# Optimization experiments

Measured on AMD Instinct MI355X. Metric: run time of the kernel, lower is better.

## Reference

```python
import jax, jax.numpy as jnp
import numpy as np
from jax import lax

N_CLASS = 21
K_ED = 5
ALPHA = 0.1
BN_EPS = 1e-5


def _conv(x, w):
    # NCHW conv, stride 1, SAME padding
    return lax.conv_general_dilated(x, w, (1, 1), 'SAME',
                                    dimension_numbers=('NCHW', 'OIHW', 'NCHW'))


def _bn(x, g, b, m, v):
    # inference-mode BatchNorm2d with running stats
    scale = (g * lax.rsqrt(v + BN_EPS))[None, :, None, None]
    return (x - m[None, :, None, None]) * scale + b[None, :, None, None]


def _maxpool(x, k):
    return lax.reduce_window(x, -jnp.inf, lax.max, (1, 1, k, k), (1, 1, 1, 1), 'SAME')


def setup_inputs() -> dict:
    key = jax.random.key(0)
    ks = jax.random.split(key, 12)
    N, F, H, W, C = 8, 512, 96, 96, N_CLASS
    feature = jax.random.normal(ks[0], (N, F, H, W), jnp.float32)
    global_pred = jax.random.normal(ks[1], (N, C, H, W), jnp.float32)
    conv1_w = jax.random.normal(ks[2], (256, F, 3, 3), jnp.float32) * 0.02
    bn1_g = jnp.ones((256,), jnp.float32)
    bn1_b = jnp.zeros((256,), jnp.float32)
    bn1_m = jax.random.normal(ks[3], (256,), jnp.float32) * 0.1
    bn1_v = jax.random.uniform(ks[4], (256,), jnp.float32, 0.5, 1.5)
    conv2_w = jax.random.normal(ks[5], (128, 256, 3, 3), jnp.float32) * 0.02
    bn2_g = jnp.ones((128,), jnp.float32)
    bn2_b = jnp.zeros((128,), jnp.float32)
    bn2_m = jax.random.normal(ks[6], (128,), jnp.float32) * 0.1
    bn2_v = jax.random.uniform(ks[7], (128,), jnp.float32, 0.5, 1.5)
    conv3_w = jax.random.normal(ks[8], (C, 128, 1, 1), jnp.float32) * 0.02
    conv3_b = jnp.zeros((C,), jnp.float32)
    return dict(feature=feature, global_pred=global_pred,
                conv1_w=conv1_w, bn1_g=bn1_g, bn1_b=bn1_b, bn1_m=bn1_m, bn1_v=bn1_v,
                conv2_w=conv2_w, bn2_g=bn2_g, bn2_b=bn2_b, bn2_m=bn2_m, bn2_v=bn2_v,
                conv3_w=conv3_w, conv3_b=conv3_b)


def reference(feature, global_pred, conv1_w, bn1_g, bn1_b, bn1_m, bn1_v,
              conv2_w, bn2_g, bn2_b, bn2_m, bn2_v, conv3_w, conv3_b):
    N, F, H, W = feature.shape
    # hard labels -> one-hot [N, C, H, W]
    lbl = jnp.argmax(global_pred, axis=1)
    onehot = jnp.transpose(jax.nn.one_hot(lbl, N_CLASS, dtype=feature.dtype), (0, 3, 1, 2))
    # binary morphology: dilation = max-pool, erosion = -max-pool(-x)
    d = _maxpool(onehot, K_ED)
    e = -_maxpool(-onehot, K_ED)
    transition = jnp.sum(d - e, axis=1, keepdims=True)
    transition = jnp.where(transition >= 1.0, 1.0, transition)  # [N,1,H,W]
    tfeat = feature * transition
    # per-class masked mean over ALL H*W pixels (faithful to .mean(dim=2))
    objs = jnp.einsum('nfhw,nchw->ncf', feature, e) / (H * W)  # [N,C,F]
    # cdist(p=2) between transition-feature pixels and class prototypes
    x = tfeat.reshape(N, F, H * W).transpose(0, 2, 1)  # [N,HW,F]
    x2 = jnp.sum(x * x, axis=-1, keepdims=True)
    o2 = jnp.sum(objs * objs, axis=-1)
    d2 = jnp.maximum(x2 + o2[:, None, :] - 2.0 * jnp.einsum('npf,ncf->npc', x, objs), 0.0)
    cd = jnp.where(d2 > 0, jnp.sqrt(jnp.where(d2 > 0, d2, 1.0)), 0.0)  # safe sqrt
    dist = 1.0 - jax.nn.softmax(cd, axis=-1)  # [N,HW,C]
    obj_feat = jnp.einsum('npc,ncf->nfp', dist, objs).reshape(N, F, H, W)
    fusion = (feature * (1.0 - transition)
              + feature * transition * ALPHA
              + obj_feat * transition * (1.0 - ALPHA))
    # fusion_predictor: convBNReLU -> bilinear x2 -> convBNReLU -> 1x1 conv
    h = jax.nn.relu(_bn(_conv(fusion, conv1_w), bn1_g, bn1_b, bn1_m, bn1_v))
    h = jax.image.resize(h, (N, 256, 2 * H, 2 * W), method='bilinear')
    h = jax.nn.relu(_bn(_conv(h, conv2_w), bn2_g, bn2_b, bn2_m, bn2_v))
    logits = _conv(h, conv3_w) + conv3_b[None, :, None, None]
    # eval mode: softmax over classes
    return jax.nn.softmax(logits, axis=1)
```

## Files before the change

### kernel.cpp

```cpp
#include <hip/hip_runtime.h>
#include <cstdint>
#include <cstddef>

typedef __attribute__((ext_vector_type(4))) float f32x4;
typedef __attribute__((ext_vector_type(8))) short short8;

__device__ __forceinline__ float bf2f(unsigned short u) {
  union { unsigned int i; float f; } x; x.i = ((unsigned int)u) << 16; return x.f;
}
__device__ __forceinline__ unsigned short f2bf(float f) {
  union { float f; unsigned int i; } x; x.f = f;
  unsigned int r = x.i + 0x7fffu + ((x.i >> 16) & 1u);
  return (unsigned short)(r >> 16);
}
__device__ __forceinline__ void gload16(unsigned short* lds, const unsigned short* g) {
  __builtin_amdgcn_global_load_lds(
      (const __attribute__((address_space(1))) unsigned int*)g,
      (__attribute__((address_space(3))) unsigned int*)lds, 16, 0, 0);
}

__global__ void k_prepbn(const float* __restrict__ g1, const float* __restrict__ b1,
                         const float* __restrict__ m1, const float* __restrict__ v1,
                         const float* __restrict__ g2, const float* __restrict__ b2,
                         const float* __restrict__ m2, const float* __restrict__ v2,
                         float* __restrict__ s1, float* __restrict__ bb1,
                         float* __restrict__ s2, float* __restrict__ bb2) {
  int i = threadIdx.x;
  if (i < 256) { float s = g1[i] * rsqrtf(v1[i] + 1e-5f); s1[i] = s; bb1[i] = b1[i] - m1[i] * s; }
  if (i < 128) { float s = g2[i] * rsqrtf(v2[i] + 1e-5f); s2[i] = s; bb2[i] = b2[i] - m2[i] * s; }
}

__global__ void k_prepw1(const float* __restrict__ w, unsigned short* __restrict__ wt) {
  int i = blockIdx.x * 256 + threadIdx.x;
  int o = i / 4608, k = i - o * 4608;
  int cblk = k / 288, r = k - cblk * 288;
  int t = r >> 5, cl = r & 31;
  int ci = cblk * 32 + cl;
  int ty = t / 3, tx = t - ty * 3;
  wt[i] = f2bf(w[((o * 512 + ci) * 3 + ty) * 3 + tx]);
}
__global__ void k_prepw2(const float* __restrict__ w, unsigned short* __restrict__ wt) {
  int i = blockIdx.x * 256 + threadIdx.x;
  int o = i / 2304, k = i - o * 2304;
  int cblk = k / 288, r = k - cblk * 288;
  int t = r >> 5, cl = r & 31;
  int ci = cblk * 32 + cl;
  int ty = t / 3, tx = t - ty * 3;
  wt[i] = f2bf(w[((o * 256 + ci) * 3 + ty) * 3 + tx]);
}
__global__ void k_prepw3(const float* __restrict__ w3, unsigned short* __restrict__ w3b) {
  int i = blockIdx.x * 256 + threadIdx.x;
  int c = i >> 7, k = i & 127;
  w3b[i] = (c < 21) ? f2bf(w3[c * 128 + k]) : (unsigned short)0;
}

template <int HP, int WP, int C>
__global__ void k_border(unsigned short* __restrict__ p) {
  const int B = 2 * WP + 2 * (HP - 2);
  const int total = 8 * B * (C / 8);
  int i = blockIdx.x * 256 + threadIdx.x;
  if (i >= total) return;
  const int cg = i % (C / 8);
  int b = i / (C / 8);
  const int n = b / B; b -= n * B;
  int y, x;
  if (b < WP) { y = 0; x = b; }
  else if (b < 2 * WP) { y = HP - 1; x = b - WP; }
  else { int r = b - 2 * WP; y = 1 + (r >> 1); x = (r & 1) ? (WP - 1) : 0; }
  short8 z = {0, 0, 0, 0, 0, 0, 0, 0};
  *(short8*)&p[(((long)n * HP + y) * WP + x) * C + cg * 8] = z;
}

__global__ __launch_bounds__(256)
void k_featT(const float* __restrict__ feat, unsigned short* __restrict__ featT) {
  const int g = blockIdx.x * 256 + threadIdx.x;
  const int n = g / 9216, p = g - n * 9216;
  const int fg0 = blockIdx.y * 16;
  const float* src = feat + (long)n * 512 * 9216 + p;
  unsigned short* dst = featT + ((long)n * 9216 + p) * 512;
  for (int fg = fg0; fg < fg0 + 16; fg++) {
    short8 o;
    #pragma unroll
    for (int j = 0; j < 8; j++) o[j] = (short)f2bf(src[(long)(fg * 8 + j) * 9216]);
    *(short8*)&dst[fg * 8] = o;
  }
}

__global__ void k_labels(const float* __restrict__ gp, signed char* __restrict__ lab) {
  int p = blockIdx.x * 256 + threadIdx.x;
  int n = p / 9216, q = p - n * 9216;
  const float* g = gp + (long)n * 21 * 9216 + q;
  float best = g[0]; int bi = 0;
  #pragma unroll
  for (int c = 1; c < 21; c++) {
    float v = g[(long)c * 9216];
    if (v > best) { best = v; bi = c; }
  }
  lab[p] = (signed char)bi;
}

__global__ void k_em(const signed char* __restrict__ lab, signed char* __restrict__ em) {
  int p = blockIdx.x * 256 + threadIdx.x;
  int n = p / 9216, q = p - n * 9216, y = q / 96, x = q - y * 96;
  const signed char* L = lab + n * 9216;
  signed char l0 = L[q];
  bool uni = true;
  for (int dy = -2; dy <= 2; dy++) {
    int yy = y + dy; if (yy < 0 || yy > 95) continue;
    for (int dx = -2; dx <= 2; dx++) {
      int xx = x + dx; if (xx < 0 || xx > 95) continue;
      uni = uni && (L[yy * 96 + xx] == l0);
    }
  }
  em[p] = uni ? l0 : (signed char)-1;
}

__global__ __launch_bounds__(256)
void k_objsT(const unsigned short* __restrict__ featT, const signed char* __restrict__ em,
             float* __restrict__ objs) {
  __shared__ float part[21 * 512];
  __shared__ signed char emL[256];
  __shared__ int pres[21];
  const int b = blockIdx.x;
  const int n = b / 36;
  const int px0 = (b - n * 36) * 256;
  const int tid = threadIdx.x;
  for (int i = tid; i < 21 * 512; i += 256) part[i] = 0.f;
  if (tid < 21) pres[tid] = 0;
  emL[tid] = em[n * 9216 + px0 + tid];
  __syncthreads();
  const unsigned short* base = featT + ((long)n * 9216 + px0) * 512 + tid * 2;
  for (int px = 0; px < 256; px++) {
    const int c0 = emL[px];
    if (c0 >= 0) {
      if (tid == 0) pres[c0] = 1;
      unsigned int v = *(const unsigned int*)&base[(long)px * 512];
      atomicAdd(&part[c0 * 512 + tid * 2], bf2f((unsigned short)(v & 0xffff)));
      atomicAdd(&part[c0 * 512 + tid * 2 + 1], bf2f((unsigned short)(v >> 16)));
    }
  }
  __syncthreads();
  for (int i = tid; i < 21 * 512; i += 256) {
    const int c = i >> 9;
    if (pres[c]) atomicAdd(&objs[(long)n * 21 * 512 + i], part[i] * (1.0f / 9216.0f));
  }
}

__global__ void k_objfin(const float* __restrict__ objs, float* __restrict__ o2,
                         unsigned short* __restrict__ oc) {
  const int b = blockIdx.x;
  const int n = b >> 5, c = b & 31;
  const int lane = threadIdx.x;
  unsigned short* dst = oc + ((long)n * 32 + c) * 512;
  if (c < 21) {
    const float* o = objs + ((long)n * 21 + c) * 512;
    float s = 0.f;
    for (int f = lane; f < 512; f += 64) {
      float v = o[f];
      s += v * v;
      dst[f] = f2bf(v);
    }
    #pragma unroll
    for (int off = 32; off; off >>= 1) s += __shfl_down(s, off);
    if (lane == 0) o2[n * 21 + c] = s;
  } else {
    for (int f = lane; f < 512; f += 64) dst[f] = 0;
  }
}

__global__ __launch_bounds__(256)
void k_dist_mfma(const unsigned short* __restrict__ featT,
                 const unsigned short* __restrict__ objs_c,
                 const float* __restrict__ o2, float* __restrict__ dist) {
  const int n = blockIdx.y;
  const int w = threadIdx.x >> 6, lane = threadIdx.x & 63;
  const int lrow = lane & 15, kg = lane >> 4;
  const int px = blockIdx.x * 64 + w * 16 + lrow;
  const unsigned short* fb = featT + ((long)n * 9216 + px) * 512 + kg * 8;
  const unsigned short* a0p = objs_c + ((long)n * 32 + lrow) * 512 + kg * 8;
  const unsigned short* a1p = a0p + 16 * 512;
  f32x4 acc0 = {0.f, 0.f, 0.f, 0.f}, acc1 = {0.f, 0.f, 0.f, 0.f};
  float x2 = 0.f;
  #pragma unroll
  for (int s = 0; s < 16; s++) {
    const short8 b = *(const short8*)&fb[s * 32];
    const short8 a0 = *(const short8*)&a0p[s * 32];
    const short8 a1 = *(const short8*)&a1p[s * 32];
    acc0 = __builtin_amdgcn_mfma_f32_16x16x32_bf16(a0, b, acc0, 0, 0, 0);
    acc1 = __builtin_amdgcn_mfma_f32_16x16x32_bf16(a1, b, acc1, 0, 0, 0);
    #pragma unroll
    for (int j = 0; j < 8; j++) { float v = bf2f((unsigned short)b[j]); x2 += v * v; }
  }
  x2 += __shfl_xor(x2, 16); x2 += __shfl_xor(x2, 32);
  float cd[8], mx = -1e30f;
  #pragma unroll
  for (int r = 0; r < 4; r++) {
    const int c = kg * 4 + r;
    float d2 = x2 + o2[n * 21 + c] - 2.f * acc0[r];
    cd[r] = sqrtf(fmaxf(d2, 0.f)); mx = fmaxf(mx, cd[r]);
  }
  #pragma unroll
  for (int r = 0; r < 4; r++) {
    const int c = 16 + kg * 4 + r;
    if (c < 21) {
      float d2 = x2 + o2[n * 21 + c] - 2.f * acc1[r];
      cd[4 + r] = sqrtf(fmaxf(d2, 0.f)); mx = fmaxf(mx, cd[4 + r]);
    } else cd[4 + r] = -1e30f;
  }
  mx = fmaxf(mx, __shfl_xor(mx, 16)); mx = fmaxf(mx, __shfl_xor(mx, 32));
  float sum = 0.f;
  #pragma unroll
  for (int k = 0; k < 8; k++) {
    cd[k] = (cd[k] > -1e29f) ? __expf(cd[k] - mx) : 0.f;
    sum += cd[k];
  }
  sum += __shfl_xor(sum, 16); sum += __shfl_xor(sum, 32);
  const float inv = 1.f / sum;
  #pragma unroll
  for (int r = 0; r < 4; r++)
    dist[((long)n * 21 + kg * 4 + r) * 9216 + px] = 1.f - cd[r] * inv;
  #pragma unroll
  for (int r = 0; r < 4; r++) {
    const int c = 16 + kg * 4 + r;
    if (c < 21) dist[((long)n * 21 + c) * 9216 + px] = 1.f - cd[4 + r] * inv;
  }
}

__global__ __launch_bounds__(256)
void k_fusion(const unsigned short* __restrict__ featT, const signed char* __restrict__ em,
              const float* __restrict__ dist, const float* __restrict__ objs,
              unsigned short* __restrict__ fuP) {
  __shared__ float ob[21 * 512];
  __shared__ float dl[64][21];
  __shared__ signed char eml[64];
  const int blk = blockIdx.x;
  const int n = blk / 144;
  const int p0 = (blk - n * 144) * 64;
  const int tid = threadIdx.x;
  for (int i = tid; i < 21 * 512; i += 256) ob[i] = objs[(long)n * 21 * 512 + i];
  for (int i = tid; i < 64 * 21; i += 256) {
    int px = i & 63, c = i >> 6;
    dl[px][c] = dist[((long)n * 21 + c) * 9216 + p0 + px];
  }
  if (tid < 64) eml[tid] = em[n * 9216 + p0 + tid];
  __syncthreads();
  const int px = tid & 63;
  const int fg = (tid >> 6) * 8;
  const int q = p0 + px;
  const int y = q / 96, x = q - y * 96;
  unsigned short* dst = fuP + (((long)n * 98 + y + 1) * 98 + (x + 1)) * 512;
  const bool t = eml[px] < 0;
  const unsigned short* srcT = featT + ((long)n * 9216 + q) * 512;
  for (int f0 = 0; f0 < 512; f0 += 32) {
    short8 o;
    const short8 fvv = *(const short8*)&srcT[f0 + fg];
    #pragma unroll
    for (int j = 0; j < 8; j++) {
      const int f = f0 + fg + j;
      float fv = bf2f((unsigned short)fvv[j]);
      if (t) {
        float of = 0.f;
        #pragma unroll
        for (int c = 0; c < 21; c++) of += dl[px][c] * ob[c * 512 + f];
        fv = 0.1f * fv + 0.9f * of;
      }
      o[j] = (short)f2bf(fv);
    }
    *(short8*)&dst[fg] = o;
    dst += 32;
  }
}

template <int CIN, int NK>
__global__ __launch_bounds__(256)
void conv3x3_gemm(const unsigned short* __restrict__ inP,
                  const unsigned short* __restrict__ wT,
                  const float* __restrict__ scale, const float* __restrict__ bias,
                  unsigned short* __restrict__ out,
                  int Hout, int Wout, int Hp, int Wp, int COUT, int nbN) {
  __shared__ unsigned short ldsA[3][4096];
  __shared__ unsigned short ldsB[3][4096];
  const int tid = threadIdx.x;
  const int chunk = gridDim.x >> 3;
  const int bid = (blockIdx.x & 7) * chunk + (blockIdx.x >> 3);
  const int mb = bid / nbN, nb = bid - mb * nbN;
  const int bm0 = mb * 128, bn0 = nb * 128;
  const int KT = 9 * CIN;
  const int HWo = Hout * Wout;

  const int rA = tid >> 2;
  const int ch8 = (((tid & 3) ^ ((tid >> 3) & 3)) * 8);
  const int m0 = bm0 + rA, m1 = m0 + 64;
  const int n0 = m0 / HWo; const int q0 = m0 - n0 * HWo;
  const int y0 = q0 / Wout, x0 = q0 - y0 * Wout;
  const int n1 = m1 / HWo; const int q1 = m1 - n1 * HWo;
  const int y1 = q1 / Wout, x1 = q1 - y1 * Wout;
  const unsigned short* gA0 = inP + ((long)(n0 * Hp + y0) * Wp + x0) * CIN + ch8;
  const unsigned short* gA1 = inP + ((long)(n1 * Hp + y1) * Wp + x1) * CIN + ch8;
  const unsigned short* gB0 = wT + (long)(bn0 + rA) * KT + ch8;
  const unsigned short* gB1 = wT + (long)(bn0 + rA + 64) * KT + ch8;

  const int lane = tid & 63;
  const int wv = tid >> 6;
  const int wr = wv >> 1, wc = wv & 1;
  const int lrow = lane & 15, kg = lane >> 4;
  const int arow = wr * 64 + lrow;
  const int aoff = arow * 32 + (kg ^ ((arow >> 1) & 3)) * 8;
  const int brow = wc * 64 + lrow;
  const int boff = brow * 32 + (kg ^ ((brow >> 1) & 3)) * 8;

  f32x4 acc[4][4];
  const f32x4 zero = {0.f, 0.f, 0.f, 0.f};
  #pragma unroll
  for (int i = 0; i < 4; i++)
    #pragma unroll
    for (int j = 0; j < 4; j++) acc[i][j] = zero;

  auto stage = [&](int b, int s) {
    const int cblk = s / 9;
    const int t = s - cblk * 9;
    const int ty = t / 3, tx = t - ty * 3;
    const long offA = (long)(ty * Wp + tx) * CIN + cblk * 32;
    gload16(&ldsA[b][tid * 8], gA0 + offA);
    gload16(&ldsA[b][2048 + tid * 8], gA1 + offA);
    const long k0 = (long)s * 32;
    gload16(&ldsB[b][tid * 8], gB0 + k0);
    gload16(&ldsB[b][2048 + tid * 8], gB1 + k0);
  };

  auto kstep = [&](int rd) {
    const unsigned short* A = ldsA[rd];
    const unsigned short* B = ldsB[rd];
    short8 af[4], bfr[4];
    #pragma unroll
    for (int i = 0; i < 4; i++) af[i] = *(const short8*)&A[aoff + i * 512];
    #pragma unroll
    for (int j = 0; j < 4; j++) bfr[j] = *(const short8*)&B[boff + j * 512];
    __builtin_amdgcn_s_setprio(1);
    #pragma unroll
    for (int i = 0; i < 4; i++)
      #pragma unroll
      for (int j = 0; j < 4; j++)
        acc[i][j] = __builtin_amdgcn_mfma_f32_16x16x32_bf16(af[i], bfr[j], acc[i][j], 0, 0, 0);
    __builtin_amdgcn_s_setprio(0);
  };

  stage(0, 0);
  stage(1, 1);
  int rd = 0, prev = 2;
  for (int s = 0; s < NK - 2; ++s) {
    __builtin_amdgcn_s_barrier();
    asm volatile("" ::: "memory");
    stage(prev, s + 2);
    asm volatile("s_waitcnt vmcnt(8)" ::: "memory");
    __builtin_amdgcn_s_barrier();
    asm volatile("" ::: "memory");
    kstep(rd);
    prev = rd; rd = (rd == 2) ? 0 : rd + 1;
  }
  asm volatile("s_waitcnt vmcnt(4)" ::: "memory");
  __builtin_amdgcn_s_barrier();
  asm volatile("" ::: "memory");
  kstep(rd);
  rd = (rd == 2) ? 0 : rd + 1;
  asm volatile("s_waitcnt vmcnt(0)" ::: "memory");
  __builtin_amdgcn_s_barrier();
  asm volatile("" ::: "memory");
  kstep(rd);

  #pragma unroll
  for (int i = 0; i < 4; i++) {
    const int row = bm0 + wr * 64 + i * 16 + kg * 4;
    #pragma unroll
    for (int j = 0; j < 4; j++) {
      const int col = bn0 + wc * 64 + j * 16 + lrow;
      const float sc = scale[col], bi = bias[col];
      #pragma unroll
      for (int r = 0; r < 4; r++) {
        float v = acc[i][j][r] * sc + bi;
        v = v > 0.f ? v : 0.f;
        out[(long)(row + r) * COUT + col] = f2bf(v);
      }
    }
  }
}

__global__ __launch_bounds__(256)
void conv2_fused(const unsigned short* __restrict__ inP,
                 const unsigned short* __restrict__ wT,
                 const float* __restrict__ scale, const float* __restrict__ bias,
                 const unsigned short* __restrict__ w3b, const float* __restrict__ b3,
                 float* __restrict__ out) {
  constexpr int CIN = 256, NK = 72;
  constexpr int Wout = 192, Hp = 194, Wp = 194;
  constexpr int HWo = 192 * 192;
  constexpr int KT = 9 * CIN;
  __shared__ unsigned short pool[6 * 4096];
  const int tid = threadIdx.x;
  const int chunk = gridDim.x >> 3;
  const int bid = (blockIdx.x & 7) * chunk + (blockIdx.x >> 3);
  const int bm0 = bid * 128;

  const int rA = tid >> 2;
  const int ch8 = (((tid & 3) ^ ((tid >> 3) & 3)) * 8);
  const int m0 = bm0 + rA, m1 = m0 + 64;
  const int n0 = m0 / HWo; const int q0 = m0 - n0 * HWo;
  const int y0 = q0 / Wout, x0 = q0 - y0 * Wout;
  const int n1 = m1 / HWo; const int q1 = m1 - n1 * HWo;
  const int y1 = q1 / Wout, x1 = q1 - y1 * Wout;
  const unsigned short* gA0 = inP + ((long)(n0 * Hp + y0) * Wp + x0) * CIN + ch8;
  const unsigned short* gA1 = inP + ((long)(n1 * Hp + y1) * Wp + x1) * CIN + ch8;
  const unsigned short* gB0 = wT + (long)rA * KT + ch8;
  const unsigned short* gB1 = wT + (long)(rA + 64) * KT + ch8;

  const int lane = tid & 63;
  const int wv = tid >> 6;
  const int wr = wv >> 1, wc = wv & 1;
  const int lrow = lane & 15, kg = lane >> 4;
  const int arow = wr * 64 + lrow;
  const int aoff = arow * 32 + (kg ^ ((arow >> 1) & 3)) * 8;
  const int brow = wc * 64 + lrow;
  const int boff = brow * 32 + (kg ^ ((brow >> 1) & 3)) * 8;

  f32x4 acc[4][4];
  const f32x4 zero = {0.f, 0.f, 0.f, 0.f};
  #pragma unroll
  for (int i = 0; i < 4; i++)
    #pragma unroll
    for (int j = 0; j < 4; j++) acc[i][j] = zero;

  auto stage = [&](int b, int s) {
    const int cblk = s / 9;
    const int t = s - cblk * 9;
    const int ty = t / 3, tx = t - ty * 3;
    const long offA = (long)(ty * Wp + tx) * CIN + cblk * 32;
    gload16(&pool[b * 4096 + tid * 8], gA0 + offA);
    gload16(&pool[b * 4096 + 2048 + tid * 8], gA1 + offA);
    const long k0 = (long)s * 32;
    gload16(&pool[12288 + b * 4096 + tid * 8], gB0 + k0);
    gload16(&pool[12288 + b * 4096 + 2048 + tid * 8], gB1 + k0);
  };

  auto kstep = [&](int rd) {
    const unsigned short* A = &pool[rd * 4096];
    const unsigned short* B = &pool[12288 + rd * 4096];
    short8 af[4], bfr[4];
    #pragma unroll
    for (int i = 0; i < 4; i++) af[i] = *(const short8*)&A[aoff + i * 512];
    #pragma unroll
    for (int j = 0; j < 4; j++) bfr[j] = *(const short8*)&B[boff + j * 512];
    __builtin_amdgcn_s_setprio(1);
    #pragma unroll
    for (int i = 0; i < 4; i++)
      #pragma unroll
      for (int j = 0; j < 4; j++)
        acc[i][j] = __builtin_amdgcn_mfma_f32_16x16x32_bf16(af[i], bfr[j], acc[i][j], 0, 0, 0);
    __builtin_amdgcn_s_setprio(0);
  };

  stage(0, 0);
  stage(1, 1);
  int rd = 0;
  for (int s = 0; s < NK; ++s) {
    if (s < NK - 1)
      asm volatile("s_waitcnt vmcnt(4)" ::: "memory");
    else
      asm volatile("s_waitcnt vmcnt(0)" ::: "memory");
    __builtin_amdgcn_s_barrier();
    asm volatile("" ::: "memory");
    kstep(rd);
    if (s + 2 < NK) stage((rd + 2 >= 3) ? rd - 1 : rd + 2, s + 2);
    rd = (rd == 2) ? 0 : rd + 1;
  }

  asm volatile("s_waitcnt lgkmcnt(0)" ::: "memory");
  __builtin_amdgcn_s_barrier();
  asm volatile("" ::: "memory");
  #pragma unroll
  for (int j = 0; j < 4; j++) {
    const int ch = wc * 64 + j * 16 + lrow;
    const float sc = scale[ch], bi = bias[ch];
    #pragma unroll
    for (int i = 0; i < 4; i++) {
      const int pxb = wr * 64 + i * 16 + kg * 4;
      #pragma unroll
      for (int r = 0; r < 4; r++) {
        const int px = pxb + r;
        float v = acc[i][j][r] * sc + bi;
        v = v > 0.f ? v : 0.f;
        pool[px * 128 + (ch ^ ((px & 7) << 3))] = f2bf(v);
      }
    }
  }
  asm volatile("s_waitcnt lgkmcnt(0)" ::: "memory");
  __builtin_amdgcn_s_barrier();
  asm volatile("" ::: "memory");

  #pragma unroll
  for (int g = 0; g < 2; g++) {
    const int px = wv * 32 + g * 16 + lrow;
    f32x4 acc0 = {0.f, 0.f, 0.f, 0.f}, acc1 = {0.f, 0.f, 0.f, 0.f};
    #pragma unroll
    for (int s = 0; s < 4; s++) {
      const int ch0 = s * 32 + kg * 8;
      const short8 b = *(const short8*)&pool[px * 128 + (ch0 ^ ((px & 7) << 3))];
      const short8 a0 = *(const short8*)&w3b[lrow * 128 + ch0];
      const short8 a1 = *(const short8*)&w3b[(16 + lrow) * 128 + ch0];
      acc0 = __builtin_amdgcn_mfma_f32_16x16x32_bf16(a0, b, acc0, 0, 0, 0);
      acc1 = __builtin_amdgcn_mfma_f32_16x16x32_bf16(a1, b, acc1, 0, 0, 0);
    }
    float lg[8], mx = -1e30f;
    #pragma unroll
    for (int r = 0; r < 4; r++) {
      lg[r] = acc0[r] + b3[kg * 4 + r];
      mx = fmaxf(mx, lg[r]);
    }
    #pragma unroll
    for (int r = 0; r < 4; r++) {
      const int c = 16 + kg * 4 + r;
      if (c < 21) { lg[4 + r] = acc1[r] + b3[c]; mx = fmaxf(mx, lg[4 + r]); }
      else lg[4 + r] = -1e30f;
    }
    mx = fmaxf(mx, __shfl_xor(mx, 16)); mx = fmaxf(mx, __shfl_xor(mx, 32));
    float sum = 0.f;
    #pragma unroll
    for (int k = 0; k < 8; k++) {
      lg[k] = (lg[k] > -1e29f) ? __expf(lg[k] - mx) : 0.f;
      sum += lg[k];
    }
    sum += __shfl_xor(sum, 16); sum += __shfl_xor(sum, 32);
    const float inv = 1.f / sum;
    const int m = bm0 + px;
    const int n = m / HWo;
    const int q = m - n * HWo;
    #pragma unroll
    for (int r = 0; r < 4; r++)
      out[((long)n * 21 + kg * 4 + r) * (long)HWo + q] = lg[r] * inv;
    #pragma unroll
    for (int r = 0; r < 4; r++) {
      const int c = 16 + kg * 4 + r;
      if (c < 21) out[((long)n * 21 + c) * (long)HWo + q] = lg[4 + r] * inv;
    }
  }
}

__global__ void k_upsample(const unsigned short* __restrict__ h1,
                           unsigned short* __restrict__ h2P) {
  const int idx = blockIdx.x * 256 + threadIdx.x;
  const int c8 = (idx & 31) * 8;
  const int p = idx >> 5;
  const int n = p / 36864; const int rr = p - n * 36864;
  const int Y = rr / 192, X = rr - Y * 192;
  const int ky = Y >> 1, kx = X >> 1;
  int yA, yB, xA, xB; float wyA, wyB, wxA, wxB;
  if ((Y & 1) == 0) { yA = ky > 0 ? ky - 1 : 0; yB = ky; wyA = 0.25f; wyB = 0.75f; }
  else { yA = ky; yB = ky < 95 ? ky + 1 : 95; wyA = 0.75f; wyB = 0.25f; }
  if ((X & 1) == 0) { xA = kx > 0 ? kx - 1 : 0; xB = kx; wxA = 0.25f; wxB = 0.75f; }
  else { xA = kx; xB = kx < 95 ? kx + 1 : 95; wxA = 0.75f; wxB = 0.25f; }
  const unsigned short* hb = h1 + (long)n * 96 * 96 * 256 + c8;
  const short8 vaa = *(const short8*)&hb[((long)yA * 96 + xA) * 256];
  const short8 vab = *(const short8*)&hb[((long)yA * 96 + xB) * 256];
  const short8 vba = *(const short8*)&hb[((long)yB * 96 + xA) * 256];
  const short8 vbb = *(const short8*)&hb[((long)yB * 96 + xB) * 256];
  short8 o;
  #pragma unroll
  for (int j = 0; j < 8; j++) {
    float v = wyA * (wxA * bf2f((unsigned short)vaa[j]) + wxB * bf2f((unsigned short)vab[j])) +
              wyB * (wxA * bf2f((unsigned short)vba[j]) + wxB * bf2f((unsigned short)vbb[j]));
    o[j] = (short)f2bf(v);
  }
  *(short8*)&h2P[(((long)n * 194 + Y + 1) * 194 + X + 1) * 256 + c8] = o;
}

extern "C" void kernel_launch(void* const* d_in, const int* in_sizes, int n_in,
                              void* d_out, int out_size, void* d_ws, size_t ws_size,
                              hipStream_t stream) {
  const float* feature = (const float*)d_in[0];
  const float* gp = (const float*)d_in[1];
  const float* w1 = (const float*)d_in[2];
  const float* g1 = (const float*)d_in[3];
  const float* b1 = (const float*)d_in[4];
  const float* m1 = (const float*)d_in[5];
  const float* v1 = (const float*)d_in[6];
  const float* w2 = (const float*)d_in[7];
  const float* g2 = (const float*)d_in[8];
  const float* b2 = (const float*)d_in[9];
  const float* m2 = (const float*)d_in[10];
  const float* v2 = (const float*)d_in[11];
  const float* w3 = (const float*)d_in[12];
  const float* b3 = (const float*)d_in[13];
  float* out = (float*)d_out;

  char* ws = (char*)d_ws;
  size_t off = 0;
  auto alloc = [&](size_t bytes) -> void* {
    void* p = ws + off;
    off += (bytes + 255) & ~(size_t)255;
    return p;
  };
  signed char* lab = (signed char*)alloc(73728);
  signed char* em = (signed char*)alloc(73728);
  float* objs = (float*)alloc(8 * 21 * 512 * 4);
  float* o2 = (float*)alloc(168 * 4);
  unsigned short* objs_c = (unsigned short*)alloc((size_t)8 * 32 * 512 * 2);
  float* dist = (float*)alloc((size_t)8 * 21 * 9216 * 4);
  unsigned short* w1t = (unsigned short*)alloc((size_t)256 * 4608 * 2);
  unsigned short* w2t = (unsigned short*)alloc((size_t)128 * 2304 * 2);
  unsigned short* w3b = (unsigned short*)alloc((size_t)32 * 128 * 2);
  float* s1 = (float*)alloc(256 * 4);
  float* bb1 = (float*)alloc(256 * 4);
  float* s2 = (float*)alloc(128 * 4);
  float* bb2 = (float*)alloc(128 * 4);
  const size_t fuP_bytes = (size_t)8 * 98 * 98 * 512 * 2;
  unsigned short* fuP = (unsigned short*)alloc(fuP_bytes);
  const size_t h1_bytes = (size_t)8 * 96 * 96 * 256 * 2;
  unsigned short* h1 = (unsigned short*)alloc(h1_bytes);
  const size_t h2P_bytes = (size_t)8 * 194 * 194 * 256 * 2;
  unsigned short* h2P = (unsigned short*)alloc(h2P_bytes);
  unsigned short* featT = h2P;

  if (off > ws_size) return;

  k_prepbn<<<1, 256, 0, stream>>>(g1, b1, m1, v1, g2, b2, m2, v2, s1, bb1, s2, bb2);
  k_prepw1<<<4608, 256, 0, stream>>>(w1, w1t);
  k_prepw2<<<1152, 256, 0, stream>>>(w2, w2t);
  k_prepw3<<<16, 256, 0, stream>>>(w3, w3b);

  k_border<98, 98, 512><<<777, 256, 0, stream>>>(fuP);
  hipMemsetAsync(objs, 0, 8 * 21 * 512 * 4, stream);

  k_labels<<<288, 256, 0, stream>>>(gp, lab);
  k_em<<<288, 256, 0, stream>>>(lab, em);
  k_featT<<<dim3(288, 4), 256, 0, stream>>>(feature, featT);
  k_objsT<<<288, 256, 0, stream>>>(featT, em, objs);
  k_objfin<<<256, 64, 0, stream>>>(objs, o2, objs_c);
  k_dist_mfma<<<dim3(144, 8), 256, 0, stream>>>(featT, objs_c, o2, dist);
  k_fusion<<<1152, 256, 0, stream>>>(featT, em, dist, objs, fuP);

  conv3x3_gemm<512, 144><<<1152, 256, 0, stream>>>(fuP, w1t, s1, bb1, h1,
                                                   96, 96, 98, 98, 256, 2);
  k_border<194, 194, 256><<<772, 256, 0, stream>>>(h2P);
  k_upsample<<<36864, 256, 0, stream>>>(h1, h2P);
  conv2_fused<<<2304, 256, 0, stream>>>(h2P, w2t, s2, bb2, w3b, b3, out);
}
```

Before: 765.3 us.

## Fuse prep, border, label, objs and dist/fusion kernels to cut launches and traffic

Merges the weight, BN and border prep kernels into single multi-role launches. The prototype accumulation moves into the feature-transpose pass, so the transposed bf16 features are not reread, and it accumulates from fp32 values instead of bf16. The distance softmax is computed inside the fusion kernel, which drops the global dist buffer round-trip. Upsample also zeros the padded border. This reduces launch count and memory traffic, at the cost of extra per-block shared-memory loads of objs and heavier LDS atomics in the transpose.

```diff
diff --git a/kernel.cpp b/kernel.cpp
--- a/kernel.cpp
+++ b/kernel.cpp
@@ -19,84 +19,74 @@
       (__attribute__((address_space(3))) unsigned int*)lds, 16, 0, 0);
 }
 
-__global__ void k_prepbn(const float* __restrict__ g1, const float* __restrict__ b1,
-                         const float* __restrict__ m1, const float* __restrict__ v1,
-                         const float* __restrict__ g2, const float* __restrict__ b2,
-                         const float* __restrict__ m2, const float* __restrict__ v2,
-                         float* __restrict__ s1, float* __restrict__ bb1,
-                         float* __restrict__ s2, float* __restrict__ bb2) {
-  int i = threadIdx.x;
-  if (i < 256) { float s = g1[i] * rsqrtf(v1[i] + 1e-5f); s1[i] = s; bb1[i] = b1[i] - m1[i] * s; }
-  if (i < 128) { float s = g2[i] * rsqrtf(v2[i] + 1e-5f); s2[i] = s; bb2[i] = b2[i] - m2[i] * s; }
-}
-
-__global__ void k_prepw1(const float* __restrict__ w, unsigned short* __restrict__ wt) {
-  int i = blockIdx.x * 256 + threadIdx.x;
-  int o = i / 4608, k = i - o * 4608;
-  int cblk = k / 288, r = k - cblk * 288;
-  int t = r >> 5, cl = r & 31;
-  int ci = cblk * 32 + cl;
-  int ty = t / 3, tx = t - ty * 3;
-  wt[i] = f2bf(w[((o * 512 + ci) * 3 + ty) * 3 + tx]);
-}
-__global__ void k_prepw2(const float* __restrict__ w, unsigned short* __restrict__ wt) {
-  int i = blockIdx.x * 256 + threadIdx.x;
-  int o = i / 2304, k = i - o * 2304;
-  int cblk = k / 288, r = k - cblk * 288;
-  int t = r >> 5, cl = r & 31;
-  int ci = cblk * 32 + cl;
-  int ty = t / 3, tx = t - ty * 3;
-  wt[i] = f2bf(w[((o * 256 + ci) * 3 + ty) * 3 + tx]);
-}
-__global__ void k_prepw3(const float* __restrict__ w3, unsigned short* __restrict__ w3b) {
-  int i = blockIdx.x * 256 + threadIdx.x;
-  int c = i >> 7, k = i & 127;
-  w3b[i] = (c < 21) ? f2bf(w3[c * 128 + k]) : (unsigned short)0;
-}
-
-template <int HP, int WP, int C>
-__global__ void k_border(unsigned short* __restrict__ p) {
-  const int B = 2 * WP + 2 * (HP - 2);
-  const int total = 8 * B * (C / 8);
-  int i = blockIdx.x * 256 + threadIdx.x;
-  if (i >= total) return;
-  const int cg = i % (C / 8);
-  int b = i / (C / 8);
-  const int n = b / B; b -= n * B;
-  int y, x;
-  if (b < WP) { y = 0; x = b; }
-  else if (b < 2 * WP) { y = HP - 1; x = b - WP; }
-  else { int r = b - 2 * WP; y = 1 + (r >> 1); x = (r & 1) ? (WP - 1) : 0; }
-  short8 z = {0, 0, 0, 0, 0, 0, 0, 0};
-  *(short8*)&p[(((long)n * HP + y) * WP + x) * C + cg * 8] = z;
-}
-
-__global__ __launch_bounds__(256)
-void k_featT(const float* __restrict__ feat, unsigned short* __restrict__ featT) {
-  const int g = blockIdx.x * 256 + threadIdx.x;
-  const int n = g / 9216, p = g - n * 9216;
-  const int fg0 = blockIdx.y * 16;
-  const float* src = feat + (long)n * 512 * 9216 + p;
-  unsigned short* dst = featT + ((long)n * 9216 + p) * 512;
-  for (int fg = fg0; fg < fg0 + 16; fg++) {
-    short8 o;
-    #pragma unroll
-    for (int j = 0; j < 8; j++) o[j] = (short)f2bf(src[(long)(fg * 8 + j) * 9216]);
-    *(short8*)&dst[fg * 8] = o;
-  }
-}
-
-__global__ void k_labels(const float* __restrict__ gp, signed char* __restrict__ lab) {
-  int p = blockIdx.x * 256 + threadIdx.x;
-  int n = p / 9216, q = p - n * 9216;
-  const float* g = gp + (long)n * 21 * 9216 + q;
-  float best = g[0]; int bi = 0;
-  #pragma unroll
-  for (int c = 1; c < 21; c++) {
-    float v = g[(long)c * 9216];
-    if (v > best) { best = v; bi = c; }
-  }
-  lab[p] = (signed char)bi;
+__global__ void k_prep(const float* __restrict__ w1, const float* __restrict__ w2,
+                       const float* __restrict__ w3,
+                       const float* __restrict__ g1, const float* __restrict__ b1,
+                       const float* __restrict__ m1, const float* __restrict__ v1,
+                       const float* __restrict__ g2, const float* __restrict__ b2,
+                       const float* __restrict__ m2, const float* __restrict__ v2,
+                       unsigned short* __restrict__ w1t, unsigned short* __restrict__ w2t,
+                       unsigned short* __restrict__ w3b,
+                       float* __restrict__ s1, float* __restrict__ bb1,
+                       float* __restrict__ s2, float* __restrict__ bb2) {
+  const int blk = blockIdx.x;
+  const int tid = threadIdx.x;
+  if (blk < 4608) {
+    int i = blk * 256 + tid;
+    int o = i / 4608, k = i - o * 4608;
+    int cblk = k / 288, r = k - cblk * 288;
+    int t = r >> 5, cl = r & 31;
+    int ci = cblk * 32 + cl;
+    int ty = t / 3, tx = t - ty * 3;
+    w1t[i] = f2bf(w1[((o * 512 + ci) * 3 + ty) * 3 + tx]);
+  } else if (blk < 5760) {
+    int i = (blk - 4608) * 256 + tid;
+    int o = i / 2304, k = i - o * 2304;
+    int cblk = k / 288, r = k - cblk * 288;
+    int t = r >> 5, cl = r & 31;
+    int ci = cblk * 32 + cl;
+    int ty = t / 3, tx = t - ty * 3;
+    w2t[i] = f2bf(w2[((o * 256 + ci) * 3 + ty) * 3 + tx]);
+  } else if (blk < 5776) {
+    int i = (blk - 5760) * 256 + tid;
+    int c = i >> 7, k = i & 127;
+    w3b[i] = (c < 21) ? f2bf(w3[c * 128 + k]) : (unsigned short)0;
+  } else {
+    if (tid < 256) { float s = g1[tid] * rsqrtf(v1[tid] + 1e-5f); s1[tid] = s; bb1[tid] = b1[tid] - m1[tid] * s; }
+    if (tid < 128) { float s = g2[tid] * rsqrtf(v2[tid] + 1e-5f); s2[tid] = s; bb2[tid] = b2[tid] - m2[tid] * s; }
+  }
+}
+
+__global__ void k_labels_init(const float* __restrict__ gp, signed char* __restrict__ lab,
+                              unsigned short* __restrict__ fuP, float* __restrict__ objs) {
+  const int blk = blockIdx.x;
+  const int tid = threadIdx.x;
+  if (blk < 288) {
+    int p = blk * 256 + tid;
+    int n = p / 9216, q = p - n * 9216;
+    const float* g = gp + (long)n * 21 * 9216 + q;
+    float best = g[0]; int bi = 0;
+    #pragma unroll
+    for (int c = 1; c < 21; c++) {
+      float v = g[(long)c * 9216];
+      if (v > best) { best = v; bi = c; }
+    }
+    lab[p] = (signed char)bi;
+  } else if (blk < 1064) {
+    int i = (blk - 288) * 256 + tid;
+    const int B = 2 * 98 + 2 * 96;
+    const int cg = i & 63; int b = i >> 6;
+    const int n = b / B; b -= n * B;
+    int y, x;
+    if (b < 98) { y = 0; x = b; }
+    else if (b < 196) { y = 97; x = b - 98; }
+    else { int r = b - 196; y = 1 + (r >> 1); x = (r & 1) ? 97 : 0; }
+    short8 z = {0, 0, 0, 0, 0, 0, 0, 0};
+    *(short8*)&fuP[(((long)n * 98 + y) * 98 + x) * 512 + cg * 8] = z;
+  } else {
+    int i = (blk - 1064) * 256 + tid;
+    objs[i] = 0.f;
+  }
 }
 
 __global__ void k_em(const signed char* __restrict__ lab, signed char* __restrict__ em) {
@@ -116,33 +106,42 @@
 }
 
 __global__ __launch_bounds__(256)
-void k_objsT(const unsigned short* __restrict__ featT, const signed char* __restrict__ em,
-             float* __restrict__ objs) {
-  __shared__ float part[21 * 512];
-  __shared__ signed char emL[256];
+void k_featT_objs(const float* __restrict__ feat, const signed char* __restrict__ em,
+                  unsigned short* __restrict__ featT, float* __restrict__ objs) {
+  __shared__ float part[21 * 128];
   __shared__ int pres[21];
-  const int b = blockIdx.x;
-  const int n = b / 36;
-  const int px0 = (b - n * 36) * 256;
+  const int g = blockIdx.x * 256 + threadIdx.x;
+  const int n = g / 9216, p = g - n * 9216;
+  const int fg0 = blockIdx.y * 16;
   const int tid = threadIdx.x;
-  for (int i = tid; i < 21 * 512; i += 256) part[i] = 0.f;
+  for (int i = tid; i < 21 * 128; i += 256) part[i] = 0.f;
   if (tid < 21) pres[tid] = 0;
-  emL[tid] = em[n * 9216 + px0 + tid];
   __syncthreads();
-  const unsigned short* base = featT + ((long)n * 9216 + px0) * 512 + tid * 2;
-  for (int px = 0; px < 256; px++) {
-    const int c0 = emL[px];
+  const int c0 = em[g];
+  if (c0 >= 0) pres[c0] = 1;
+  const float* src = feat + (long)n * 512 * 9216 + p;
+  unsigned short* dst = featT + ((long)n * 9216 + p) * 512;
+  for (int fg = fg0; fg < fg0 + 16; fg++) {
+    short8 o;
+    float fv[8];
+    #pragma unroll
+    for (int j = 0; j < 8; j++) {
+      fv[j] = src[(long)(fg * 8 + j) * 9216];
+      o[j] = (short)f2bf(fv[j]);
+    }
+    *(short8*)&dst[fg * 8] = o;
     if (c0 >= 0) {
-      if (tid == 0) pres[c0] = 1;
-      unsigned int v = *(const unsigned int*)&base[(long)px * 512];
-      atomicAdd(&part[c0 * 512 + tid * 2], bf2f((unsigned short)(v & 0xffff)));
-      atomicAdd(&part[c0 * 512 + tid * 2 + 1], bf2f((unsigned short)(v >> 16)));
+      const int lf0 = (fg - fg0) * 8;
+      #pragma unroll
+      for (int j = 0; j < 8; j++) atomicAdd(&part[c0 * 128 + lf0 + j], fv[j]);
     }
   }
   __syncthreads();
-  for (int i = tid; i < 21 * 512; i += 256) {
-    const int c = i >> 9;
-    if (pres[c]) atomicAdd(&objs[(long)n * 21 * 512 + i], part[i] * (1.0f / 9216.0f));
+  for (int i = tid; i < 21 * 128; i += 256) {
+    const int c = i >> 7, lf = i & 127;
+    if (pres[c])
+      atomicAdd(&objs[((long)n * 21 + c) * 512 + blockIdx.y * 128 + lf],
+                part[i] * (1.0f / 9216.0f));
   }
 }
 
@@ -169,13 +168,24 @@
 }
 
 __global__ __launch_bounds__(256)
-void k_dist_mfma(const unsigned short* __restrict__ featT,
-                 const unsigned short* __restrict__ objs_c,
-                 const float* __restrict__ o2, float* __restrict__ dist) {
+void k_dist_fusion(const unsigned short* __restrict__ featT,
+                   const unsigned short* __restrict__ objs_c,
+                   const float* __restrict__ o2, const float* __restrict__ objs,
+                   const signed char* __restrict__ em,
+                   unsigned short* __restrict__ fuP) {
+  __shared__ float ob[21 * 512];
+  __shared__ float dl[64][21];
+  __shared__ signed char eml[64];
   const int n = blockIdx.y;
-  const int w = threadIdx.x >> 6, lane = threadIdx.x & 63;
+  const int p0 = blockIdx.x * 64;
+  const int tid = threadIdx.x;
+  const int w = tid >> 6, lane = tid & 63;
   const int lrow = lane & 15, kg = lane >> 4;
-  const int px = blockIdx.x * 64 + w * 16 + lrow;
+
+  for (int i = tid; i < 21 * 512; i += 256) ob[i] = objs[(long)n * 21 * 512 + i];
+  if (tid < 64) eml[tid] = em[n * 9216 + p0 + tid];
+
+  const int px = p0 + w * 16 + lrow;
   const unsigned short* fb = featT + ((long)n * 9216 + px) * 512 + kg * 8;
   const unsigned short* a0p = objs_c + ((long)n * 32 + lrow) * 512 + kg * 8;
   const unsigned short* a1p = a0p + 16 * 512;
@@ -216,40 +226,22 @@
   }
   sum += __shfl_xor(sum, 16); sum += __shfl_xor(sum, 32);
   const float inv = 1.f / sum;
-  #pragma unroll
-  for (int r = 0; r < 4; r++)
-    dist[((long)n * 21 + kg * 4 + r) * 9216 + px] = 1.f - cd[r] * inv;
+  const int lpx = w * 16 + lrow;
+  #pragma unroll
+  for (int r = 0; r < 4; r++) dl[lpx][kg * 4 + r] = 1.f - cd[r] * inv;
   #pragma unroll
   for (int r = 0; r < 4; r++) {
     const int c = 16 + kg * 4 + r;
-    if (c < 21) dist[((long)n * 21 + c) * 9216 + px] = 1.f - cd[4 + r] * inv;
-  }
-}
-
-__global__ __launch_bounds__(256)
-void k_fusion(const unsigned short* __restrict__ featT, const signed char* __restrict__ em,
-              const float* __restrict__ dist, const float* __restrict__ objs,
-              unsigned short* __restrict__ fuP) {
-  __shared__ float ob[21 * 512];
-  __shared__ float dl[64][21];
-  __shared__ signed char eml[64];
-  const int blk = blockIdx.x;
-  const int n = blk / 144;
-  const int p0 = (blk - n * 144) * 64;
-  const int tid = threadIdx.x;
-  for (int i = tid; i < 21 * 512; i += 256) ob[i] = objs[(long)n * 21 * 512 + i];
-  for (int i = tid; i < 64 * 21; i += 256) {
-    int px = i & 63, c = i >> 6;
-    dl[px][c] = dist[((long)n * 21 + c) * 9216 + p0 + px];
-  }
-  if (tid < 64) eml[tid] = em[n * 9216 + p0 + tid];
+    if (c < 21) dl[lpx][c] = 1.f - cd[4 + r] * inv;
+  }
   __syncthreads();
-  const int px = tid & 63;
+
+  const int px2 = tid & 63;
   const int fg = (tid >> 6) * 8;
-  const int q = p0 + px;
+  const int q = p0 + px2;
   const int y = q / 96, x = q - y * 96;
   unsigned short* dst = fuP + (((long)n * 98 + y + 1) * 98 + (x + 1)) * 512;
-  const bool t = eml[px] < 0;
+  const bool t = eml[px2] < 0;
   const unsigned short* srcT = featT + ((long)n * 9216 + q) * 512;
   for (int f0 = 0; f0 < 512; f0 += 32) {
     short8 o;
@@ -261,7 +253,7 @@
       if (t) {
         float of = 0.f;
         #pragma unroll
-        for (int c = 0; c < 21; c++) of += dl[px][c] * ob[c * 512 + f];
+        for (int c = 0; c < 21; c++) of += dl[px2][c] * ob[c * 512 + f];
         fv = 0.1f * fv + 0.9f * of;
       }
       o[j] = (short)f2bf(fv);
@@ -546,6 +538,19 @@
 
 __global__ void k_upsample(const unsigned short* __restrict__ h1,
                            unsigned short* __restrict__ h2P) {
+  if (blockIdx.x >= 36864) {
+    int i = (blockIdx.x - 36864) * 256 + threadIdx.x;
+    const int B = 2 * 194 + 2 * 192;
+    const int cg = i & 31; int b = i >> 5;
+    const int n = b / B; b -= n * B;
+    int y, x;
+    if (b < 194) { y = 0; x = b; }
+    else if (b < 388) { y = 193; x = b - 194; }
+    else { int r = b - 388; y = 1 + (r >> 1); x = (r & 1) ? 193 : 0; }
+    short8 z = {0, 0, 0, 0, 0, 0, 0, 0};
+    *(short8*)&h2P[(((long)n * 194 + y) * 194 + x) * 256 + cg * 8] = z;
+    return;
+  }
   const int idx = blockIdx.x * 256 + threadIdx.x;
   const int c8 = (idx & 31) * 8;
   const int p = idx >> 5;
@@ -603,7 +608,6 @@
   float* objs = (float*)alloc(8 * 21 * 512 * 4);
   float* o2 = (float*)alloc(168 * 4);
   unsigned short* objs_c = (unsigned short*)alloc((size_t)8 * 32 * 512 * 2);
-  float* dist = (float*)alloc((size_t)8 * 21 * 9216 * 4);
   unsigned short* w1t = (unsigned short*)alloc((size_t)256 * 4608 * 2);
   unsigned short* w2t = (unsigned short*)alloc((size_t)128 * 2304 * 2);
   unsigned short* w3b = (unsigned short*)alloc((size_t)32 * 128 * 2);
@@ -621,25 +625,16 @@
 
   if (off > ws_size) return;
 
-  k_prepbn<<<1, 256, 0, stream>>>(g1, b1, m1, v1, g2, b2, m2, v2, s1, bb1, s2, bb2);
-  k_prepw1<<<4608, 256, 0, stream>>>(w1, w1t);
-  k_prepw2<<<1152, 256, 0, stream>>>(w2, w2t);
-  k_prepw3<<<16, 256, 0, stream>>>(w3, w3b);
-
-  k_border<98, 98, 512><<<777, 256, 0, stream>>>(fuP);
-  hipMemsetAsync(objs, 0, 8 * 21 * 512 * 4, stream);
-
-  k_labels<<<288, 256, 0, stream>>>(gp, lab);
+  k_prep<<<5777, 256, 0, stream>>>(w1, w2, w3, g1, b1, m1, v1, g2, b2, m2, v2,
+                                   w1t, w2t, w3b, s1, bb1, s2, bb2);
+  k_labels_init<<<1400, 256, 0, stream>>>(gp, lab, fuP, objs);
   k_em<<<288, 256, 0, stream>>>(lab, em);
-  k_featT<<<dim3(288, 4), 256, 0, stream>>>(feature, featT);
-  k_objsT<<<288, 256, 0, stream>>>(featT, em, objs);
+  k_featT_objs<<<dim3(288, 4), 256, 0, stream>>>(feature, em, featT, objs);
   k_objfin<<<256, 64, 0, stream>>>(objs, o2, objs_c);
-  k_dist_mfma<<<dim3(144, 8), 256, 0, stream>>>(featT, objs_c, o2, dist);
-  k_fusion<<<1152, 256, 0, stream>>>(featT, em, dist, objs, fuP);
+  k_dist_fusion<<<dim3(144, 8), 256, 0, stream>>>(featT, objs_c, o2, objs, em, fuP);
 
   conv3x3_gemm<512, 144><<<1152, 256, 0, stream>>>(fuP, w1t, s1, bb1, h1,
                                                    96, 96, 98, 98, 256, 2);
-  k_border<194, 194, 256><<<772, 256, 0, stream>>>(h2P);
-  k_upsample<<<36864, 256, 0, stream>>>(h1, h2P);
+  k_upsample<<<37636, 256, 0, stream>>>(h1, h2P);
   conv2_fused<<<2304, 256, 0, stream>>>(h2P, w2t, s2, bb2, w3b, b3, out);
 }
```

Result: faster. 720.8 us (median of 2 runs) (-5.8%).
